# Kernel tuning notes

Hardware: AMD Instinct MI355X
Metric: run time of the kernel (lower is better)

Reference implementation:

```python
import jax, jax.numpy as jnp
import numpy as np
import math

B, N, WIDTH, HEADS = 2, 2048, 1024, 16
ATTN_CH = WIDTH // HEADS  # 64 (note: width//heads//3 of the 3*width fused dim)


def setup_inputs() -> dict:
    key = jax.random.key(0)
    ks = jax.random.split(key, 3)
    std = 0.02
    return {
        "x": jax.random.normal(ks[0], (B, N, WIDTH), dtype=jnp.float32),
        "w_qkv": jax.random.normal(ks[1], (WIDTH, 3 * WIDTH), dtype=jnp.float32) * std,
        "b_qkv": jnp.zeros((3 * WIDTH,), dtype=jnp.float32),
        "w_proj": jax.random.normal(ks[2], (WIDTH, WIDTH), dtype=jnp.float32) * std,
        "b_proj": jnp.zeros((WIDTH,), dtype=jnp.float32),
    }


def reference(x, w_qkv, b_qkv, w_proj, b_proj):
    bs, n_ctx, width = x.shape
    qkv = x @ w_qkv + b_qkv                       # [b, n, 3*width]
    attn_ch = (3 * width) // HEADS // 3           # head dim
    scale = 1.0 / math.sqrt(math.sqrt(attn_ch))
    # per-head layout: [b, n, heads, 3*attn_ch] -> split q,k,v
    qkv = qkv.reshape(bs, n_ctx, HEADS, 3 * attn_ch)
    q, k, v = jnp.split(qkv, 3, axis=-1)          # each [b, n, h, c]
    weight = jnp.einsum("bthc,bshc->bhts", q * scale, k * scale)
    weight = jax.nn.softmax(weight.astype(jnp.float32), axis=-1).astype(qkv.dtype)
    out = jnp.einsum("bhts,bshc->bthc", weight, v).reshape(bs, n_ctx, -1)
    return out @ w_proj + b_proj
```

## Files before the change

kernel.cpp:

```cpp
#include <hip/hip_runtime.h>
#include <hip/hip_fp16.h>

#define BATCH 2
#define NCTX  2048
#define WIDTH 1024
#define HEADS 16
#define CH    64
#define QKVD  (3 * WIDTH)
#define MROWS (BATCH * NCTX)

typedef __attribute__((ext_vector_type(4))) float    f32x4;
typedef __attribute__((ext_vector_type(8))) _Float16 f16x8;

__device__ __forceinline__ void gll16(void* lds, const void* g) {
    __builtin_amdgcn_global_load_lds(
        (const __attribute__((address_space(1))) unsigned int*)g,
        (__attribute__((address_space(3))) unsigned int*)lds, 16, 0, 0);
}

__global__ __launch_bounds__(256)
void split_x_f16(const float* __restrict__ x, __half* __restrict__ tiles)
{
    const int mb = blockIdx.x, kt = blockIdx.y;
    const int t = threadIdx.x;
    __half* tb = (__half*)tiles + ((size_t)mb * 32 + kt) * 4096;
    #pragma unroll
    for (int it = 0; it < 2; ++it) {
        const int idx = it * 256 + t;
        const int m = idx >> 2, q = idx & 3;
        const float* src = x + (size_t)(mb * 128 + m) * WIDTH + kt * 32 + q * 8;
        const f32x4 v0 = *(const f32x4*)src;
        const f32x4 v1 = *(const f32x4*)(src + 4);
        f16x8 h;
        #pragma unroll
        for (int j = 0; j < 4; ++j) { h[j] = (_Float16)v0[j]; h[4 + j] = (_Float16)v1[j]; }
        *(f16x8*)&tb[(q * 128 + m) * 8] = h;
    }
}

__global__ __launch_bounds__(256)
void split_w_f16(const float* __restrict__ w, __half* __restrict__ tiles, int N)
{
    __shared__ float tile[32][129];
    const int nb = blockIdx.x, kt = blockIdx.y;
    const int t = threadIdx.x;
    #pragma unroll
    for (int it = 0; it < 2; ++it) {
        const int idx = it * 256 + t;
        const int kk = idx >> 4, n8 = idx & 15;
        const float* src = w + (size_t)(kt * 32 + kk) * N + nb * 128 + n8 * 8;
        #pragma unroll
        for (int j = 0; j < 8; ++j) tile[kk][n8 * 8 + j] = src[j];
    }
    __syncthreads();
    __half* tb = tiles + ((size_t)nb * 32 + kt) * 4096;
    #pragma unroll
    for (int it = 0; it < 2; ++it) {
        const int idx = it * 256 + t;
        const int q = idx >> 7, nn = idx & 127;
        f16x8 h;
        #pragma unroll
        for (int j = 0; j < 8; ++j) h[j] = (_Float16)tile[q * 8 + j][nn];
        *(f16x8*)&tb[(q * 128 + nn) * 8] = h;
    }
}

__global__ __launch_bounds__(256)
void gemm_qkv(const __half* __restrict__ At, const __half* __restrict__ Bt,
              const float* __restrict__ bias,
              __half* __restrict__ qg, __half* __restrict__ kg, __half* __restrict__ vtg)
{
    __shared__ __align__(16) _Float16 sm[8192];
    const int t = threadIdx.x, lane = t & 63, w = t >> 6;
    const int lq = lane & 15, quad = lane >> 4;
    const int nb = blockIdx.x, mb = blockIdx.y;
    const int wm = (w >> 1) * 64, wn = (w & 1) * 64;

    const __half* Ab = At + ((size_t)mb * 32) * 4096;
    const __half* Bb = Bt + ((size_t)nb * 32) * 4096;

    f32x4 acc[4][4];
    #pragma unroll
    for (int i = 0; i < 4; ++i)
        #pragma unroll
        for (int j = 0; j < 4; ++j) acc[i][j] = 0;

    for (int kt = 0; kt < 32; ++kt) {
        __syncthreads();
        #pragma unroll
        for (int i = 0; i < 4; ++i) {
            const int c = w * 4 + i;
            void* lds = (void*)&sm[c * 512];
            const __half* g = (c < 8 ? Ab + (size_t)kt * 4096 + c * 512
                                     : Bb + (size_t)kt * 4096 + (c - 8) * 512) + lane * 8;
            gll16(lds, g);
        }
        __syncthreads();

        f16x8 a[4], b[4];
        #pragma unroll
        for (int i = 0; i < 4; ++i) {
            a[i] = *(const f16x8*)&sm[(quad * 128 + wm + i * 16 + lq) * 8];
            b[i] = *(const f16x8*)&sm[4096 + (quad * 128 + wn + i * 16 + lq) * 8];
        }
        #pragma unroll
        for (int i = 0; i < 4; ++i)
            #pragma unroll
            for (int j = 0; j < 4; ++j)
                acc[i][j] = __builtin_amdgcn_mfma_f32_16x16x32_f16(a[i], b[j], acc[i][j], 0, 0, 0);
    }

    const int bb = mb >> 4;
    #pragma unroll
    for (int jf = 0; jf < 4; ++jf) {
        const int col = nb * 128 + wn + jf * 16 + lq;
        const int h = col / 192;
        const int sect = col - h * 192;
        const int type = sect >> 6;
        const int c = sect & 63;
        const float bv = bias[col];
        const size_t bh = (size_t)bb * 16 + h;
        #pragma unroll
        for (int i = 0; i < 4; ++i) {
            #pragma unroll
            for (int r = 0; r < 4; ++r) {
                const int n = (mb & 15) * 128 + wm + i * 16 + quad * 4 + r;
                const float v = acc[i][jf][r] + bv;
                if (type == 0) {
                    const size_t a2 = ((bh * 16 + (n >> 7)) * 8 + (c >> 3)) * 1024
                                      + (size_t)(n & 127) * 8 + (c & 7);
                    qg[a2] = __float2half(v * 0.125f);
                } else if (type == 1) {
                    const size_t a2 = ((bh * 32 + (n >> 6)) * 8 + (c >> 3)) * 512
                                      + (size_t)(n & 63) * 8 + (c & 7);
                    kg[a2] = __float2half(v);
                } else {
                    const size_t a2 = ((bh * 32 + (n >> 6)) * 8 + ((n >> 3) & 7)) * 512
                                      + (size_t)c * 8 + (n & 7);
                    vtg[a2] = __float2half(v);
                }
            }
        }
    }
}

__global__ __launch_bounds__(256)
void attn_mfma2(const __half* __restrict__ qg, const __half* __restrict__ kg,
                const __half* __restrict__ vtg, __half* __restrict__ a2)
{
    __shared__ __align__(16) _Float16 Ks[4096];
    __shared__ __align__(16) _Float16 Vt[4096];
    __shared__ __align__(16) _Float16 Ps[8192];

    const int t = threadIdx.x, lane = t & 63, w = t >> 6;
    const int lq = lane & 15, quad = lane >> 4;
    const int bid = blockIdx.x;
    const int qt2 = bid & 15, h = (bid >> 4) & 15, b = bid >> 8;
    const size_t bh = (size_t)b * 16 + h;

    const __half* qtile = qg + (bh * 16 + qt2) * 8192;
    const __half* kbase = kg + bh * 32 * 4096;
    const __half* vbase = vtg + bh * 32 * 4096;

    #pragma unroll
    for (int i = 0; i < 4; ++i)
        gll16((void*)&Ps[(w * 4 + i) * 512], (const void*)(qtile + (w * 4 + i) * 512 + lane * 8));
    __syncthreads();

    f16x8 aq[2][2];
    #pragma unroll
    for (int qn = 0; qn < 2; ++qn)
        #pragma unroll
        for (int ks = 0; ks < 2; ++ks)
            aq[qn][ks] = *(const f16x8*)&Ps[((ks * 4 + quad) * 128 + w * 32 + qn * 16 + lq) * 8];

    f32x4 O[2][4];
    #pragma unroll
    for (int qn = 0; qn < 2; ++qn)
        #pragma unroll
        for (int j = 0; j < 4; ++j) O[qn][j] = 0;
    float lpart[2] = {0.0f, 0.0f};

    _Float16* Pw = &Ps[w * 2048];
    const int kb_hi = quad >> 1, joff = (quad & 1) * 4;

    for (int kt = 0; kt < 32; ++kt) {
        __syncthreads();
        #pragma unroll
        for (int i = 0; i < 2; ++i) {
            gll16((void*)&Ks[(w * 2 + i) * 512],
                  (const void*)(kbase + (size_t)kt * 4096 + (w * 2 + i) * 512 + lane * 8));
            gll16((void*)&Vt[(w * 2 + i) * 512],
                  (const void*)(vbase + (size_t)kt * 4096 + (w * 2 + i) * 512 + lane * 8));
        }
        __syncthreads();

        f32x4 st[4][2];
        #pragma unroll
        for (int mt = 0; mt < 4; ++mt) { st[mt][0] = 0; st[mt][1] = 0; }
        #pragma unroll
        for (int ks = 0; ks < 2; ++ks)
            #pragma unroll
            for (int mt = 0; mt < 4; ++mt) {
                f16x8 kf = *(const f16x8*)&Ks[((ks * 4 + quad) * 64 + mt * 16 + lq) * 8];
                st[mt][0] = __builtin_amdgcn_mfma_f32_16x16x32_f16(kf, aq[0][ks], st[mt][0], 0, 0, 0);
                st[mt][1] = __builtin_amdgcn_mfma_f32_16x16x32_f16(kf, aq[1][ks], st[mt][1], 0, 0, 0);
            }

        #pragma unroll
        for (int mt = 0; mt < 4; ++mt) {
            #pragma unroll
            for (int qn = 0; qn < 2; ++qn) {
                const float e0 = __expf(st[mt][qn][0]);
                const float e1 = __expf(st[mt][qn][1]);
                const float e2 = __expf(st[mt][qn][2]);
                const float e3 = __expf(st[mt][qn][3]);
                lpart[qn] += (e0 + e1) + (e2 + e3);
                __half2 p01 = __floats2half2_rn(e0, e1);
                __half2 p23 = __floats2half2_rn(e2, e3);
                uint2 pk;
                pk.x = *(unsigned*)&p01;
                pk.y = *(unsigned*)&p23;
                *(uint2*)&Pw[((mt * 2 + kb_hi) * 32 + qn * 16 + lq) * 8 + joff] = pk;
            }
        }
        asm volatile("s_waitcnt lgkmcnt(0)" ::: "memory");

        #pragma unroll
        for (int ks = 0; ks < 2; ++ks) {
            f16x8 ap0 = *(const f16x8*)&Pw[((ks * 4 + quad) * 32 + lq) * 8];
            f16x8 ap1 = *(const f16x8*)&Pw[((ks * 4 + quad) * 32 + 16 + lq) * 8];
            #pragma unroll
            for (int jc = 0; jc < 4; ++jc) {
                f16x8 vf = *(const f16x8*)&Vt[((ks * 4 + quad) * 64 + jc * 16 + lq) * 8];
                O[0][jc] = __builtin_amdgcn_mfma_f32_16x16x32_f16(ap0, vf, O[0][jc], 0, 0, 0);
                O[1][jc] = __builtin_amdgcn_mfma_f32_16x16x32_f16(ap1, vf, O[1][jc], 0, 0, 0);
            }
        }
    }

    float linv[2][4];
    #pragma unroll
    for (int qn = 0; qn < 2; ++qn) {
        float v = lpart[qn];
        v += __shfl_xor(v, 16);
        v += __shfl_xor(v, 32);
        #pragma unroll
        for (int r = 0; r < 4; ++r)
            linv[qn][r] = 1.0f / __shfl(v, quad * 4 + r);
    }
    __half* a2t = a2 + ((size_t)b * 16 + qt2) * 32 * 4096;
    #pragma unroll
    for (int jc = 0; jc < 4; ++jc) {
        const int ch = h * 64 + jc * 16 + lq;
        const int ktp = ch >> 5;
        const int qc = (ch >> 3) & 3;
        const int j = ch & 7;
        #pragma unroll
        for (int qn = 0; qn < 2; ++qn)
            #pragma unroll
            for (int r = 0; r < 4; ++r) {
                const int m = w * 32 + qn * 16 + quad * 4 + r;
                a2t[(size_t)ktp * 4096 + (qc * 128 + m) * 8 + j] =
                    __float2half(O[qn][jc][r] * linv[qn][r]);
            }
    }
}

__global__ __launch_bounds__(256)
void gemm_proj(const __half* __restrict__ At, const __half* __restrict__ Bt,
               const float* __restrict__ bias, float* __restrict__ out)
{
    __shared__ __align__(16) _Float16 sm[8192];
    const int t = threadIdx.x, lane = t & 63, w = t >> 6;
    const int lq = lane & 15, quad = lane >> 4;
    const int nb = blockIdx.x, mb = blockIdx.y;
    const int wm = (w >> 1) * 64, wn = (w & 1) * 64;

    const __half* Ab = At + ((size_t)mb * 32) * 4096;
    const __half* Bb = Bt + ((size_t)nb * 32) * 4096;

    f32x4 acc[4][4];
    #pragma unroll
    for (int i = 0; i < 4; ++i)
        #pragma unroll
        for (int j = 0; j < 4; ++j) acc[i][j] = 0;

    for (int kt = 0; kt < 32; ++kt) {
        __syncthreads();
        #pragma unroll
        for (int i = 0; i < 4; ++i) {
            const int c = w * 4 + i;
            void* lds = (void*)&sm[c * 512];
            const __half* g = (c < 8 ? Ab + (size_t)kt * 4096 + c * 512
                                     : Bb + (size_t)kt * 4096 + (c - 8) * 512) + lane * 8;
            gll16(lds, g);
        }
        __syncthreads();

        f16x8 a[4], b[4];
        #pragma unroll
        for (int i = 0; i < 4; ++i) {
            a[i] = *(const f16x8*)&sm[(quad * 128 + wm + i * 16 + lq) * 8];
            b[i] = *(const f16x8*)&sm[4096 + (quad * 128 + wn + i * 16 + lq) * 8];
        }
        #pragma unroll
        for (int i = 0; i < 4; ++i)
            #pragma unroll
            for (int j = 0; j < 4; ++j)
                acc[i][j] = __builtin_amdgcn_mfma_f32_16x16x32_f16(a[i], b[j], acc[i][j], 0, 0, 0);
    }

    #pragma unroll
    for (int jf = 0; jf < 4; ++jf) {
        const int col = nb * 128 + wn + jf * 16 + lq;
        const float bv = bias[col];
        #pragma unroll
        for (int i = 0; i < 4; ++i)
            #pragma unroll
            for (int r = 0; r < 4; ++r) {
                const int row = mb * 128 + wm + i * 16 + quad * 4 + r;
                out[(size_t)row * WIDTH + col] = acc[i][jf][r] + bv;
            }
    }
}

extern "C" void kernel_launch(void* const* d_in, const int* in_sizes, int n_in,
                              void* d_out, int out_size, void* d_ws, size_t ws_size,
                              hipStream_t stream)
{
    const float* x      = (const float*)d_in[0];
    const float* w_qkv  = (const float*)d_in[1];
    const float* b_qkv  = (const float*)d_in[2];
    const float* w_proj = (const float*)d_in[3];
    const float* b_proj = (const float*)d_in[4];
    float* out = (float*)d_out;

    char* p = (char*)d_ws;
    size_t o = 0;
    __half* A1  = (__half*)(p + o); o += (size_t)MROWS * WIDTH * 2;
    __half* Bq  = (__half*)(p + o); o += (size_t)WIDTH * QKVD * 2;
    __half* Qg  = (__half*)(p + o); o += (size_t)MROWS * WIDTH * 2;
    __half* Kg  = (__half*)(p + o); o += (size_t)MROWS * WIDTH * 2;
    __half* Vtg = (__half*)(p + o); o += (size_t)MROWS * WIDTH * 2;
    __half* A2  = (__half*)(p + o); o += (size_t)MROWS * WIDTH * 2;
    __half* Bp  = (__half*)(p + o); o += (size_t)WIDTH * WIDTH * 2;

    dim3 blk(256);

    split_x_f16<<<dim3(32, 32), blk, 0, stream>>>(x, A1);
    split_w_f16<<<dim3(24, 32), blk, 0, stream>>>(w_qkv, Bq, QKVD);
    split_w_f16<<<dim3(8, 32),  blk, 0, stream>>>(w_proj, Bp, WIDTH);

    gemm_qkv<<<dim3(24, 32), blk, 0, stream>>>(A1, Bq, b_qkv, Qg, Kg, Vtg);

    attn_mfma2<<<dim3(512), blk, 0, stream>>>(Qg, Kg, Vtg, A2);

    gemm_proj<<<dim3(8, 32), blk, 0, stream>>>(A2, Bp, b_proj, out);
}
```

Baseline: 220.2 us.

## Double-buffer LDS tiles with register prefetch in GEMMs and attention

```diff
diff --git a/kernel.cpp b/kernel.cpp
--- a/kernel.cpp
+++ b/kernel.cpp
@@ -70,7 +70,7 @@
               const float* __restrict__ bias,
               __half* __restrict__ qg, __half* __restrict__ kg, __half* __restrict__ vtg)
 {
-    __shared__ __align__(16) _Float16 sm[8192];
+    __shared__ __align__(16) _Float16 sm[16384];
     const int t = threadIdx.x, lane = t & 63, w = t >> 6;
     const int lq = lane & 15, quad = lane >> 4;
     const int nb = blockIdx.x, mb = blockIdx.y;
@@ -78,6 +78,7 @@
 
     const __half* Ab = At + ((size_t)mb * 32) * 4096;
     const __half* Bb = Bt + ((size_t)nb * 32) * 4096;
+    const int c0 = w * 4;
 
     f32x4 acc[4][4];
     #pragma unroll
@@ -85,29 +86,50 @@
         #pragma unroll
         for (int j = 0; j < 4; ++j) acc[i][j] = 0;
 
+    f16x8 pf[4];
+    #pragma unroll
+    for (int i = 0; i < 4; ++i) {
+        const int c = c0 + i;
+        const __half* g = (c < 8 ? Ab + c * 512 : Bb + (c - 8) * 512) + lane * 8;
+        pf[i] = *(const f16x8*)g;
+    }
+    #pragma unroll
+    for (int i = 0; i < 4; ++i)
+        *(f16x8*)&sm[(c0 + i) * 512 + lane * 8] = pf[i];
+    __syncthreads();
+
     for (int kt = 0; kt < 32; ++kt) {
-        __syncthreads();
+        _Float16* cur = sm + (kt & 1) * 8192;
+        _Float16* nxt = sm + ((kt + 1) & 1) * 8192;
+
+        if (kt + 1 < 32) {
+            #pragma unroll
+            for (int i = 0; i < 4; ++i) {
+                const int c = c0 + i;
+                const __half* g = (c < 8 ? Ab + (size_t)(kt + 1) * 4096 + c * 512
+                                         : Bb + (size_t)(kt + 1) * 4096 + (c - 8) * 512) + lane * 8;
+                pf[i] = *(const f16x8*)g;
+            }
+        }
+
+        f16x8 a[4], b[4];
         #pragma unroll
         for (int i = 0; i < 4; ++i) {
-            const int c = w * 4 + i;
-            void* lds = (void*)&sm[c * 512];
-            const __half* g = (c < 8 ? Ab + (size_t)kt * 4096 + c * 512
-                                     : Bb + (size_t)kt * 4096 + (c - 8) * 512) + lane * 8;
-            gll16(lds, g);
-        }
-        __syncthreads();
-
-        f16x8 a[4], b[4];
-        #pragma unroll
-        for (int i = 0; i < 4; ++i) {
-            a[i] = *(const f16x8*)&sm[(quad * 128 + wm + i * 16 + lq) * 8];
-            b[i] = *(const f16x8*)&sm[4096 + (quad * 128 + wn + i * 16 + lq) * 8];
+            a[i] = *(const f16x8*)&cur[(quad * 128 + wm + i * 16 + lq) * 8];
+            b[i] = *(const f16x8*)&cur[4096 + (quad * 128 + wn + i * 16 + lq) * 8];
         }
         #pragma unroll
         for (int i = 0; i < 4; ++i)
             #pragma unroll
             for (int j = 0; j < 4; ++j)
                 acc[i][j] = __builtin_amdgcn_mfma_f32_16x16x32_f16(a[i], b[j], acc[i][j], 0, 0, 0);
+
+        if (kt + 1 < 32) {
+            #pragma unroll
+            for (int i = 0; i < 4; ++i)
+                *(f16x8*)&nxt[(c0 + i) * 512 + lane * 8] = pf[i];
+        }
+        __syncthreads();
     }
 
     const int bb = mb >> 4;
@@ -148,8 +170,8 @@
 void attn_mfma2(const __half* __restrict__ qg, const __half* __restrict__ kg,
                 const __half* __restrict__ vtg, __half* __restrict__ a2)
 {
-    __shared__ __align__(16) _Float16 Ks[4096];
-    __shared__ __align__(16) _Float16 Vt[4096];
+    __shared__ __align__(16) _Float16 Ks[2][4096];
+    __shared__ __align__(16) _Float16 Vt[2][4096];
     __shared__ __align__(16) _Float16 Ps[8192];
 
     const int t = threadIdx.x, lane = t & 63, w = t >> 6;
@@ -165,14 +187,27 @@
     #pragma unroll
     for (int i = 0; i < 4; ++i)
         gll16((void*)&Ps[(w * 4 + i) * 512], (const void*)(qtile + (w * 4 + i) * 512 + lane * 8));
+
+    f16x8 pf[4];
+    #pragma unroll
+    for (int i = 0; i < 2; ++i) {
+        pf[i]     = *(const f16x8*)(kbase + (w * 2 + i) * 512 + lane * 8);
+        pf[2 + i] = *(const f16x8*)(vbase + (w * 2 + i) * 512 + lane * 8);
+    }
     __syncthreads();
 
+    #pragma unroll
+    for (int i = 0; i < 2; ++i) {
+        *(f16x8*)&Ks[0][(w * 2 + i) * 512 + lane * 8] = pf[i];
+        *(f16x8*)&Vt[0][(w * 2 + i) * 512 + lane * 8] = pf[2 + i];
+    }
     f16x8 aq[2][2];
     #pragma unroll
     for (int qn = 0; qn < 2; ++qn)
         #pragma unroll
         for (int ks = 0; ks < 2; ++ks)
             aq[qn][ks] = *(const f16x8*)&Ps[((ks * 4 + quad) * 128 + w * 32 + qn * 16 + lq) * 8];
+    __syncthreads();
 
     f32x4 O[2][4];
     #pragma unroll
@@ -185,15 +220,15 @@
     const int kb_hi = quad >> 1, joff = (quad & 1) * 4;
 
     for (int kt = 0; kt < 32; ++kt) {
-        __syncthreads();
-        #pragma unroll
-        for (int i = 0; i < 2; ++i) {
-            gll16((void*)&Ks[(w * 2 + i) * 512],
-                  (const void*)(kbase + (size_t)kt * 4096 + (w * 2 + i) * 512 + lane * 8));
-            gll16((void*)&Vt[(w * 2 + i) * 512],
-                  (const void*)(vbase + (size_t)kt * 4096 + (w * 2 + i) * 512 + lane * 8));
-        }
-        __syncthreads();
+        const int cur = kt & 1, nxtb = (kt + 1) & 1;
+
+        if (kt + 1 < 32) {
+            #pragma unroll
+            for (int i = 0; i < 2; ++i) {
+                pf[i]     = *(const f16x8*)(kbase + (size_t)(kt + 1) * 4096 + (w * 2 + i) * 512 + lane * 8);
+                pf[2 + i] = *(const f16x8*)(vbase + (size_t)(kt + 1) * 4096 + (w * 2 + i) * 512 + lane * 8);
+            }
+        }
 
         f32x4 st[4][2];
         #pragma unroll
@@ -202,7 +237,7 @@
         for (int ks = 0; ks < 2; ++ks)
             #pragma unroll
             for (int mt = 0; mt < 4; ++mt) {
-                f16x8 kf = *(const f16x8*)&Ks[((ks * 4 + quad) * 64 + mt * 16 + lq) * 8];
+                f16x8 kf = *(const f16x8*)&Ks[cur][((ks * 4 + quad) * 64 + mt * 16 + lq) * 8];
                 st[mt][0] = __builtin_amdgcn_mfma_f32_16x16x32_f16(kf, aq[0][ks], st[mt][0], 0, 0, 0);
                 st[mt][1] = __builtin_amdgcn_mfma_f32_16x16x32_f16(kf, aq[1][ks], st[mt][1], 0, 0, 0);
             }
@@ -232,11 +267,20 @@
             f16x8 ap1 = *(const f16x8*)&Pw[((ks * 4 + quad) * 32 + 16 + lq) * 8];
             #pragma unroll
             for (int jc = 0; jc < 4; ++jc) {
-                f16x8 vf = *(const f16x8*)&Vt[((ks * 4 + quad) * 64 + jc * 16 + lq) * 8];
+                f16x8 vf = *(const f16x8*)&Vt[cur][((ks * 4 + quad) * 64 + jc * 16 + lq) * 8];
                 O[0][jc] = __builtin_amdgcn_mfma_f32_16x16x32_f16(ap0, vf, O[0][jc], 0, 0, 0);
                 O[1][jc] = __builtin_amdgcn_mfma_f32_16x16x32_f16(ap1, vf, O[1][jc], 0, 0, 0);
             }
         }
+
+        if (kt + 1 < 32) {
+            #pragma unroll
+            for (int i = 0; i < 2; ++i) {
+                *(f16x8*)&Ks[nxtb][(w * 2 + i) * 512 + lane * 8] = pf[i];
+                *(f16x8*)&Vt[nxtb][(w * 2 + i) * 512 + lane * 8] = pf[2 + i];
+            }
+        }
+        __syncthreads();
     }
 
     float linv[2][4];
@@ -271,7 +315,7 @@
 void gemm_proj(const __half* __restrict__ At, const __half* __restrict__ Bt,
                const float* __restrict__ bias, float* __restrict__ out)
 {
-    __shared__ __align__(16) _Float16 sm[8192];
+    __shared__ __align__(16) _Float16 sm[16384];
     const int t = threadIdx.x, lane = t & 63, w = t >> 6;
     const int lq = lane & 15, quad = lane >> 4;
     const int nb = blockIdx.x, mb = blockIdx.y;
@@ -279,6 +323,7 @@
 
     const __half* Ab = At + ((size_t)mb * 32) * 4096;
     const __half* Bb = Bt + ((size_t)nb * 32) * 4096;
+    const int c0 = w * 4;
 
     f32x4 acc[4][4];
     #pragma unroll
@@ -286,29 +331,50 @@
         #pragma unroll
         for (int j = 0; j < 4; ++j) acc[i][j] = 0;
 
+    f16x8 pf[4];
+    #pragma unroll
+    for (int i = 0; i < 4; ++i) {
+        const int c = c0 + i;
+        const __half* g = (c < 8 ? Ab + c * 512 : Bb + (c - 8) * 512) + lane * 8;
+        pf[i] = *(const f16x8*)g;
+    }
+    #pragma unroll
+    for (int i = 0; i < 4; ++i)
+        *(f16x8*)&sm[(c0 + i) * 512 + lane * 8] = pf[i];
+    __syncthreads();
+
     for (int kt = 0; kt < 32; ++kt) {
-        __syncthreads();
+        _Float16* cur = sm + (kt & 1) * 8192;
+        _Float16* nxt = sm + ((kt + 1) & 1) * 8192;
+
+        if (kt + 1 < 32) {
+            #pragma unroll
+            for (int i = 0; i < 4; ++i) {
+                const int c = c0 + i;
+                const __half* g = (c < 8 ? Ab + (size_t)(kt + 1) * 4096 + c * 512
+                                         : Bb + (size_t)(kt + 1) * 4096 + (c - 8) * 512) + lane * 8;
+                pf[i] = *(const f16x8*)g;
+            }
+        }
+
+        f16x8 a[4], b[4];
         #pragma unroll
         for (int i = 0; i < 4; ++i) {
-            const int c = w * 4 + i;
-            void* lds = (void*)&sm[c * 512];
-            const __half* g = (c < 8 ? Ab + (size_t)kt * 4096 + c * 512
-                                     : Bb + (size_t)kt * 4096 + (c - 8) * 512) + lane * 8;
-            gll16(lds, g);
-        }
-        __syncthreads();
-
-        f16x8 a[4], b[4];
-        #pragma unroll
-        for (int i = 0; i < 4; ++i) {
-            a[i] = *(const f16x8*)&sm[(quad * 128 + wm + i * 16 + lq) * 8];
-            b[i] = *(const f16x8*)&sm[4096 + (quad * 128 + wn + i * 16 + lq) * 8];
+            a[i] = *(const f16x8*)&cur[(quad * 128 + wm + i * 16 + lq) * 8];
+            b[i] = *(const f16x8*)&cur[4096 + (quad * 128 + wn + i * 16 + lq) * 8];
         }
         #pragma unroll
         for (int i = 0; i < 4; ++i)
             #pragma unroll
             for (int j = 0; j < 4; ++j)
                 acc[i][j] = __builtin_amdgcn_mfma_f32_16x16x32_f16(a[i], b[j], acc[i][j], 0, 0, 0);
+
+        if (kt + 1 < 32) {
+            #pragma unroll
+            for (int i = 0; i < 4; ++i)
+                *(f16x8*)&nxt[(c0 + i) * 512 + lane * 8] = pf[i];
+        }
+        __syncthreads();
     }
 
     #pragma unroll
```

Measured after the change: 205.4 us. 6.7% less time.
